# Performance work log

Hardware: AMD Instinct MI355X
Metric: run time of the kernel (lower is better)

Reference implementation:

```python
import jax, jax.numpy as jnp
import numpy as np

LN_EPS = 1e-5

def _layernorm(x, g, b):
    mu = jnp.mean(x, axis=-1, keepdims=True)
    var = jnp.mean(jnp.square(x - mu), axis=-1, keepdims=True)
    return (x - mu) * jax.lax.rsqrt(var + LN_EPS) * g + b

def setup_inputs() -> dict:
    key = jax.random.key(0)
    B, IN_DIM, S, D = 16384, 512, 32, 128
    ks = jax.random.split(key, 6)
    return {
        "x": jax.random.normal(ks[0], (B, IN_DIM), dtype=jnp.float32),
        "memory": jax.random.normal(ks[1], (1, S, D), dtype=jnp.float32),
        "ln_g": jnp.ones((IN_DIM,), dtype=jnp.float32),
        "ln_b": jnp.zeros((IN_DIM,), dtype=jnp.float32),
        "w_in": jax.random.normal(ks[2], (IN_DIM, D), dtype=jnp.float32) * 0.02,
        "b_in": jnp.zeros((D,), dtype=jnp.float32),
        "w_gate": jax.random.normal(ks[3], (2 * D, D), dtype=jnp.float32) * 0.02,
        "b_gate": jnp.zeros((D,), dtype=jnp.float32),
    }

def reference(x, memory, ln_g, ln_b, w_in, b_in, w_gate, b_gate):
    B = x.shape[0]
    mem = memory[0]                                   # [S, D]
    S, D = mem.shape
    x_proj = _layernorm(x, ln_g, ln_b) @ w_in + b_in  # [B, D]
    scores = x_proj @ mem.T                           # [B, S]
    probs = jax.nn.softmax(scores, axis=-1)           # [B, S]
    # read path
    read_content = probs @ mem                        # [B, D]
    # write path
    mem_b = jnp.broadcast_to(mem, (B, S, D))
    xp_b = jnp.broadcast_to(x_proj[:, None, :], (B, S, D))
    gate_in = jnp.concatenate([mem_b, xp_b], axis=-1)              # [B, S, 2D]
    update_gate = jax.nn.sigmoid(gate_in @ w_gate + b_gate)        # [B, S, D]
    write_info = probs[:, :, None] * x_proj[:, None, :]            # [B, S, D]
    avg_gate = jnp.mean(update_gate, axis=0, keepdims=True)        # [1, S, D]
    avg_write = jnp.mean(write_info, axis=0, keepdims=True)        # [1, S, D]
    new_memory = memory * (1.0 - avg_gate) + avg_write * avg_gate  # [1, S, D]
    return read_content, jax.lax.stop_gradient(new_memory)
```

## Files before the change

### kernel.cpp

```cpp
#include <hip/hip_runtime.h>
#include <stdint.h>

typedef __attribute__((ext_vector_type(8))) short bfrag_t;
typedef __attribute__((ext_vector_type(4))) float floatx4;

#define WFRAG_OFF   0
#define GB_OFF      294912
#define BU_OFF      311296
#define BS_OFF      311808
#define MEMFRAG_OFF 311936
#define ACC_OFF     327680
#define NBLK        512

#define M_A     0
#define M_XPF   32768
#define M_U     40960
#define M_SC    57344
#define M_PR    61440
#define M_PRT   63488
#define M_LDS   65536

__device__ __forceinline__ unsigned short f2bf(float f) {
    unsigned u = __float_as_uint(f);
    u += 0x7fffu + ((u >> 16) & 1u);
    return (unsigned short)(u >> 16);
}
__device__ __forceinline__ float sigm(float v) {
    return __builtin_amdgcn_rcpf(1.0f + __expf(-v));
}
__device__ __forceinline__ void writefrag(unsigned short* wf, int k, int n, float v) {
    int kt = k >> 5, kk = k & 31;
    int lane = (n & 15) | ((kk >> 3) << 4);
    wf[(((kt * 18) + (n >> 4)) * 64 + lane) * 8 + (kk & 7)] = f2bf(v);
}

__global__ __launch_bounds__(256) void prep_kernel(
    const float* __restrict__ memv, const float* __restrict__ w_in,
    const float* __restrict__ b_in, const float* __restrict__ w_gate,
    const float* __restrict__ b_gate, unsigned char* __restrict__ ws)
{
    int bid = blockIdx.x, t = threadIdx.x;
    unsigned short* wfrag = (unsigned short*)(ws + WFRAG_OFF);
    const float* wg2 = w_gate + 128 * 128;

    if (bid < 256) {
        __shared__ float wrow[2][128];
        int k0 = bid * 2;
        wrow[t >> 7][t & 127] = w_in[(size_t)(k0 + (t >> 7)) * 128 + (t & 127)];
        __syncthreads();
        for (int kl = 0; kl < 2; ++kl) {
            int k = k0 + kl;
            float v;
            if (t < 128) {
                v = wrow[kl][t];
            } else {
                int d = t - 128;
                float acc = 0.f;
                #pragma unroll 16
                for (int j = 0; j < 128; ++j) acc += wrow[kl][j] * wg2[j * 128 + d];
                v = acc;
            }
            writefrag(wfrag, k, t, v);
            if (t < 32) {
                float acc = 0.f;
                #pragma unroll 16
                for (int d = 0; d < 128; ++d) acc += wrow[kl][d] * memv[t * 128 + d];
                writefrag(wfrag, k, 256 + t, acc);
            }
        }
    } else if (bid < 272) {
        int idx = (bid - 256) * 256 + t;
        int s = idx >> 7, d = idx & 127;
        float acc = b_gate[d];
        #pragma unroll 16
        for (int k = 0; k < 128; ++k) acc += memv[s * 128 + k] * w_gate[k * 128 + d];
        ((float*)(ws + GB_OFF))[idx] = acc;
    } else {
        if (t < 128) {
            float acc = 0.f;
            #pragma unroll 16
            for (int j = 0; j < 128; ++j) acc += b_in[j] * wg2[j * 128 + t];
            ((float*)(ws + BU_OFF))[t] = acc;
        }
        if (t < 32) {
            float acc = 0.f;
            #pragma unroll 16
            for (int d = 0; d < 128; ++d) acc += b_in[d] * memv[t * 128 + d];
            ((float*)(ws + BS_OFF))[t] = acc;
        }
        unsigned short* mfr = (unsigned short*)(ws + MEMFRAG_OFF);
        for (int idx = t; idx < 4096; idx += 256) {
            int s = idx >> 7, d = idx & 127;
            mfr[((d >> 4) * 64 + ((d & 15) | (((s >> 3) & 3) << 4))) * 8 + (s & 7)]
                = f2bf(memv[idx]);
        }
    }
}

__global__ __launch_bounds__(512, 4) void main_kernel(
    const float* __restrict__ x,
    const float* __restrict__ ln_g, const float* __restrict__ ln_b,
    const float* __restrict__ b_in, unsigned char* __restrict__ ws,
    float* __restrict__ out)
{
    __shared__ char smem[M_LDS] __attribute__((aligned(16)));

    int tid = threadIdx.x;
    int w = tid >> 6, l = tid & 63;
    int lane_lo = l & 15, lane_hi = l >> 4;
    int row_base = blockIdx.x * 32;

    int nf = (w < 2) ? 3 : 2;
    int nts[3] = {w, w + 8, 16 + w};
    const bfrag_t* wf = (const bfrag_t*)(ws + WFRAG_OFF);

    const float4* x4 = (const float4*)x;
    float4 g0 = ((const float4*)ln_g)[l];
    float4 g1 = ((const float4*)ln_g)[l + 64];
    float4 q0 = ((const float4*)ln_b)[l];
    float4 q1 = ((const float4*)ln_b)[l + 64];

    float4 xa[4], xb[4];
    #pragma unroll
    for (int i = 0; i < 4; ++i) {
        int r = w * 4 + i;
        xa[i] = x4[(size_t)(row_base + r) * 128 + l];
        xb[i] = x4[(size_t)(row_base + r) * 128 + 64 + l];
    }

    bfrag_t bcur[3], bnxt[3], bfar[3];
    #pragma unroll
    for (int i = 0; i < 3; ++i) {
        if (i < nf) {
            bcur[i] = wf[(0 * 18 + nts[i]) * 64 + l];
            bnxt[i] = wf[(1 * 18 + nts[i]) * 64 + l];
        }
    }
    float bin_v = b_in[w * 16 + lane_lo];
    float bu_v  = ((const float*)(ws + BU_OFF))[w * 16 + lane_lo];
    float bs_v  = (w < 2) ? ((const float*)(ws + BS_OFF))[w * 16 + lane_lo] : 0.f;

    #pragma unroll
    for (int i = 0; i < 4; ++i) {
        int r = w * 4 + i;
        float s1 = xa[i].x + xa[i].y + xa[i].z + xa[i].w + xb[i].x + xb[i].y + xb[i].z + xb[i].w;
        float s2 = xa[i].x*xa[i].x + xa[i].y*xa[i].y + xa[i].z*xa[i].z + xa[i].w*xa[i].w
                 + xb[i].x*xb[i].x + xb[i].y*xb[i].y + xb[i].z*xb[i].z + xb[i].w*xb[i].w;
        #pragma unroll
        for (int m = 1; m < 64; m <<= 1) {
            s1 += __shfl_xor(s1, m);
            s2 += __shfl_xor(s2, m);
        }
        float mu = s1 * (1.f / 512.f);
        float var = s2 * (1.f / 512.f) - mu * mu;
        float rs = rsqrtf(var + 1e-5f);
        float ya0 = (xa[i].x - mu) * rs * g0.x + q0.x;
        float ya1 = (xa[i].y - mu) * rs * g0.y + q0.y;
        float ya2 = (xa[i].z - mu) * rs * g0.z + q0.z;
        float ya3 = (xa[i].w - mu) * rs * g0.w + q0.w;
        float yb0 = (xb[i].x - mu) * rs * g1.x + q1.x;
        float yb1 = (xb[i].y - mu) * rs * g1.y + q1.y;
        float yb2 = (xb[i].z - mu) * rs * g1.z + q1.z;
        float yb3 = (xb[i].w - mu) * rs * g1.w + q1.w;
        unsigned long long pa =
            (unsigned long long)f2bf(ya0) | ((unsigned long long)f2bf(ya1) << 16) |
            ((unsigned long long)f2bf(ya2) << 32) | ((unsigned long long)f2bf(ya3) << 48);
        unsigned long long pb =
            (unsigned long long)f2bf(yb0) | ((unsigned long long)f2bf(yb1) << 16) |
            ((unsigned long long)f2bf(yb2) << 32) | ((unsigned long long)f2bf(yb3) << 48);
        int sw = (r & 7) << 4;
        *(unsigned long long*)(smem + M_A + ((r * 1024 + l * 8) ^ sw)) = pa;
        *(unsigned long long*)(smem + M_A + ((r * 1024 + 512 + l * 8) ^ sw)) = pb;
    }
    __syncthreads();

    int swa = (l & 7) << 4;
    int ab0 = lane_lo * 1024 + (lane_hi << 4);
    int ab1 = (16 + lane_lo) * 1024 + (lane_hi << 4);

    floatx4 acc[3][2];
    #pragma unroll
    for (int i = 0; i < 3; ++i)
        #pragma unroll
        for (int mt = 0; mt < 2; ++mt)
            acc[i][mt] = (floatx4){0.f, 0.f, 0.f, 0.f};

    bfrag_t acur0, acur1, anxt0, anxt1, afar0, afar1;
    acur0 = *(const bfrag_t*)(smem + M_A + (ab0 ^ swa));
    acur1 = *(const bfrag_t*)(smem + M_A + (ab1 ^ swa));
    anxt0 = *(const bfrag_t*)(smem + M_A + ((ab0 + 64) ^ swa));
    anxt1 = *(const bfrag_t*)(smem + M_A + ((ab1 + 64) ^ swa));

    for (int kt = 0; kt < 16; ++kt) {
        if (kt < 14) {
            int ko = (kt + 2) * 64;
            afar0 = *(const bfrag_t*)(smem + M_A + ((ab0 + ko) ^ swa));
            afar1 = *(const bfrag_t*)(smem + M_A + ((ab1 + ko) ^ swa));
            #pragma unroll
            for (int i = 0; i < 3; ++i)
                if (i < nf) bfar[i] = wf[((kt + 2) * 18 + nts[i]) * 64 + l];
        }
        #pragma unroll
        for (int i = 0; i < 3; ++i) {
            if (i < nf) {
                acc[i][0] = __builtin_amdgcn_mfma_f32_16x16x32_bf16(acur0, bcur[i], acc[i][0], 0, 0, 0);
                acc[i][1] = __builtin_amdgcn_mfma_f32_16x16x32_bf16(acur1, bcur[i], acc[i][1], 0, 0, 0);
            }
        }
        acur0 = anxt0; acur1 = anxt1; anxt0 = afar0; anxt1 = afar1;
        #pragma unroll
        for (int i = 0; i < 3; ++i)
            if (i < nf) { bcur[i] = bnxt[i]; bnxt[i] = bfar[i]; }
    }

    {
        #pragma unroll
        for (int i = 0; i < 3; ++i) {
            if (i < nf) {
                int n = nts[i] * 16 + lane_lo;
                float bias = (i == 0) ? bin_v : ((i == 1) ? bu_v : bs_v);
                #pragma unroll
                for (int mt = 0; mt < 2; ++mt) {
                    #pragma unroll
                    for (int r4 = 0; r4 < 4; ++r4) {
                        int row = mt * 16 + lane_hi * 4 + r4;
                        float v = acc[i][mt][r4] + bias;
                        if (i == 0) {
                            int addr = M_XPF +
                                (((n >> 4) * 64 + ((n & 15) | ((row >> 3) << 4))) * 8
                                 + (row & 7)) * 2;
                            *(unsigned short*)(smem + addr) = f2bf(v);
                        } else if (i == 1) {
                            int d = n - 128;
                            *(float*)(smem + M_U + (row * 128 + d) * 4) = v;
                        } else {
                            int s = n - 256;
                            *(float*)(smem + M_SC + (row * 32 + s) * 4) = v;
                        }
                    }
                }
            }
        }
    }
    __syncthreads();

    bfrag_t bm = ((const bfrag_t*)(ws + MEMFRAG_OFF))[w * 64 + l];
    bfrag_t bx = *(const bfrag_t*)(smem + M_XPF + (w * 64 + l) * 16);
    int sbase = w * 4;
    const float* gb = (const float*)(ws + GB_OFF);
    float gbr0[4], gbr1[4];
    #pragma unroll
    for (int si = 0; si < 4; ++si) {
        gbr0[si] = gb[(sbase + si) * 128 + l];
        gbr1[si] = gb[(sbase + si) * 128 + l + 64];
    }

    #pragma unroll
    for (int i = 0; i < 4; ++i) {
        int r = w * 4 + i;
        int s = l & 31;
        float sc = *(const float*)(smem + M_SC + (r * 32 + s) * 4);
        float mx = sc;
        #pragma unroll
        for (int m = 1; m < 32; m <<= 1) mx = fmaxf(mx, __shfl_xor(mx, m));
        float e = __expf(sc - mx);
        float sum = e;
        #pragma unroll
        for (int m = 1; m < 32; m <<= 1) sum += __shfl_xor(sum, m);
        float p = e * __builtin_amdgcn_rcpf(sum);
        if (l < 32) {
            unsigned short pb = f2bf(p);
            *(unsigned short*)(smem + M_PR +
                (((r >> 4) * 64 + ((r & 15) + 16 * (s >> 3))) * 8 + (s & 7)) * 2) = pb;
            *(unsigned short*)(smem + M_PRT +
                (((s >> 4) * 64 + ((s & 15) + 16 * (r >> 3))) * 8 + (r & 7)) * 2) = pb;
        }
    }
    __syncthreads();

    float* pw = (float*)(ws + ACC_OFF + (size_t)blockIdx.x * 32768);
    {
        bfrag_t pa0 = *(const bfrag_t*)(smem + M_PR + l * 16);
        bfrag_t pa1 = *(const bfrag_t*)(smem + M_PR + 1024 + l * 16);
        bfrag_t pat0 = *(const bfrag_t*)(smem + M_PRT + l * 16);
        bfrag_t pat1 = *(const bfrag_t*)(smem + M_PRT + 1024 + l * 16);

        floatx4 r0 = (floatx4){0.f, 0.f, 0.f, 0.f};
        floatx4 r1 = (floatx4){0.f, 0.f, 0.f, 0.f};
        r0 = __builtin_amdgcn_mfma_f32_16x16x32_bf16(pa0, bm, r0, 0, 0, 0);
        r1 = __builtin_amdgcn_mfma_f32_16x16x32_bf16(pa1, bm, r1, 0, 0, 0);
        floatx4 w0 = (floatx4){0.f, 0.f, 0.f, 0.f};
        floatx4 w1 = (floatx4){0.f, 0.f, 0.f, 0.f};
        w0 = __builtin_amdgcn_mfma_f32_16x16x32_bf16(pat0, bx, w0, 0, 0, 0);
        w1 = __builtin_amdgcn_mfma_f32_16x16x32_bf16(pat1, bx, w1, 0, 0, 0);

        int nc = w * 16 + lane_lo;
        #pragma unroll
        for (int r4 = 0; r4 < 4; ++r4) {
            int row = lane_hi * 4 + r4;
            out[(size_t)(row_base + row) * 128 + nc] = r0[r4];
            out[(size_t)(row_base + row + 16) * 128 + nc] = r1[r4];
            pw[row * 128 + nc] = w0[r4];
            pw[(row + 16) * 128 + nc] = w1[r4];
        }
    }

    {
        float* pg = pw + 4096;
        float ag0[4], ag1[4];
        #pragma unroll
        for (int si = 0; si < 4; ++si) { ag0[si] = 0.f; ag1[si] = 0.f; }
        #pragma unroll 4
        for (int r = 0; r < 32; ++r) {
            float uv0 = *(const float*)(smem + M_U + (r * 128 + l) * 4);
            float uv1 = *(const float*)(smem + M_U + (r * 128 + l + 64) * 4);
            #pragma unroll
            for (int si = 0; si < 4; ++si) {
                ag0[si] += sigm(gbr0[si] + uv0);
                ag1[si] += sigm(gbr1[si] + uv1);
            }
        }
        #pragma unroll
        for (int si = 0; si < 4; ++si) {
            pg[(sbase + si) * 128 + l]      = ag0[si];
            pg[(sbase + si) * 128 + l + 64] = ag1[si];
        }
    }
}

__global__ __launch_bounds__(512) void fin_kernel(
    const float* __restrict__ memv, const unsigned char* __restrict__ ws,
    float* __restrict__ out2)
{
    __shared__ float4 red[2][32][16];
    int b = blockIdx.x, t = threadIdx.x;
    int f4 = t & 15, ch = t >> 4;
    const float* base = (const float*)(ws + ACC_OFF);
    int e4 = b * 16 + f4;

    float4 aw = {0.f, 0.f, 0.f, 0.f}, ag = {0.f, 0.f, 0.f, 0.f};
    #pragma unroll 4
    for (int c = ch * 16; c < ch * 16 + 16; ++c) {
        float4 a = ((const float4*)(base + (size_t)c * 8192))[e4];
        float4 g = ((const float4*)(base + (size_t)c * 8192 + 4096))[e4];
        aw.x += a.x; aw.y += a.y; aw.z += a.z; aw.w += a.w;
        ag.x += g.x; ag.y += g.y; ag.z += g.z; ag.w += g.w;
    }
    red[0][ch][f4] = aw;
    red[1][ch][f4] = ag;
    __syncthreads();
    if (t < 16) {
        float4 a = {0.f, 0.f, 0.f, 0.f}, g = {0.f, 0.f, 0.f, 0.f};
        #pragma unroll
        for (int c = 0; c < 32; ++c) {
            float4 ra = red[0][c][t], rg = red[1][c][t];
            a.x += ra.x; a.y += ra.y; a.z += ra.z; a.w += ra.w;
            g.x += rg.x; g.y += rg.y; g.z += rg.z; g.w += rg.w;
        }
        const float4 m4 = ((const float4*)memv)[b * 16 + t];
        float4 o;
        float s = 1.f / 16384.f;
        float gx = g.x * s, gy = g.y * s, gz = g.z * s, gw = g.w * s;
        o.x = m4.x * (1.f - gx) + a.x * s * gx;
        o.y = m4.y * (1.f - gy) + a.y * s * gy;
        o.z = m4.z * (1.f - gz) + a.z * s * gz;
        o.w = m4.w * (1.f - gw) + a.w * s * gw;
        ((float4*)out2)[b * 16 + t] = o;
    }
}

extern "C" void kernel_launch(void* const* d_in, const int* in_sizes, int n_in,
                              void* d_out, int out_size, void* d_ws, size_t ws_size,
                              hipStream_t stream)
{
    (void)in_sizes; (void)n_in; (void)out_size; (void)ws_size;
    const float* x      = (const float*)d_in[0];
    const float* memv   = (const float*)d_in[1];
    const float* ln_g   = (const float*)d_in[2];
    const float* ln_b   = (const float*)d_in[3];
    const float* w_in   = (const float*)d_in[4];
    const float* b_in   = (const float*)d_in[5];
    const float* w_gate = (const float*)d_in[6];
    const float* b_gate = (const float*)d_in[7];
    float* out = (float*)d_out;
    unsigned char* ws = (unsigned char*)d_ws;

    hipLaunchKernelGGL(prep_kernel, dim3(273), dim3(256), 0, stream,
                       memv, w_in, b_in, w_gate, b_gate, ws);
    hipLaunchKernelGGL(main_kernel, dim3(NBLK), dim3(512), 0, stream,
                       x, ln_g, ln_b, b_in, ws, out);
    hipLaunchKernelGGL(fin_kernel, dim3(64), dim3(512), 0, stream,
                       memv, ws, out + 2097152);
}
```

Before: 49.15 us.

## Store per-block partial sums as bf16 and restructure final reduction

Per-block write and gate partial accumulators are now stored as bf16 instead of fp32, halving workspace traffic between the main and final kernels. The final reduction kernel is rewritten so each thread loads one block's 16-column slice and reduces across the block with wave shuffles, using 256 blocks instead of 64. Half of the gate sigmoid accumulation loop is moved before the softmax section, likely to overlap its latency with other work. Rounding the partial sums to bf16 loses precision in the averaged memory update.

```diff
diff --git a/kernel.cpp b/kernel.cpp
--- a/kernel.cpp
+++ b/kernel.cpp
@@ -3,6 +3,7 @@
 
 typedef __attribute__((ext_vector_type(8))) short bfrag_t;
 typedef __attribute__((ext_vector_type(4))) float floatx4;
+typedef __attribute__((ext_vector_type(8))) unsigned short ushort8_t;
 
 #define WFRAG_OFF   0
 #define GB_OFF      294912
@@ -24,6 +25,9 @@
     unsigned u = __float_as_uint(f);
     u += 0x7fffu + ((u >> 16) & 1u);
     return (unsigned short)(u >> 16);
+}
+__device__ __forceinline__ float bf2f(unsigned short h) {
+    return __uint_as_float(((unsigned)h) << 16);
 }
 __device__ __forceinline__ float sigm(float v) {
     return __builtin_amdgcn_rcpf(1.0f + __expf(-v));
@@ -255,6 +259,20 @@
         gbr1[si] = gb[(sbase + si) * 128 + l + 64];
     }
 
+    float ag0[4], ag1[4];
+    #pragma unroll
+    for (int si = 0; si < 4; ++si) { ag0[si] = 0.f; ag1[si] = 0.f; }
+    #pragma unroll 4
+    for (int r = 0; r < 16; ++r) {
+        float uv0 = *(const float*)(smem + M_U + (r * 128 + l) * 4);
+        float uv1 = *(const float*)(smem + M_U + (r * 128 + l + 64) * 4);
+        #pragma unroll
+        for (int si = 0; si < 4; ++si) {
+            ag0[si] += sigm(gbr0[si] + uv0);
+            ag1[si] += sigm(gbr1[si] + uv1);
+        }
+    }
+
     #pragma unroll
     for (int i = 0; i < 4; ++i) {
         int r = w * 4 + i;
@@ -278,7 +296,7 @@
     }
     __syncthreads();
 
-    float* pw = (float*)(ws + ACC_OFF + (size_t)blockIdx.x * 32768);
+    unsigned short* pwh = (unsigned short*)(ws + ACC_OFF + (size_t)blockIdx.x * 16384);
     {
         bfrag_t pa0 = *(const bfrag_t*)(smem + M_PR + l * 16);
         bfrag_t pa1 = *(const bfrag_t*)(smem + M_PR + 1024 + l * 16);
@@ -300,18 +318,14 @@
             int row = lane_hi * 4 + r4;
             out[(size_t)(row_base + row) * 128 + nc] = r0[r4];
             out[(size_t)(row_base + row + 16) * 128 + nc] = r1[r4];
-            pw[row * 128 + nc] = w0[r4];
-            pw[(row + 16) * 128 + nc] = w1[r4];
+            pwh[row * 128 + nc] = f2bf(w0[r4]);
+            pwh[(row + 16) * 128 + nc] = f2bf(w1[r4]);
         }
     }
 
     {
-        float* pg = pw + 4096;
-        float ag0[4], ag1[4];
-        #pragma unroll
-        for (int si = 0; si < 4; ++si) { ag0[si] = 0.f; ag1[si] = 0.f; }
         #pragma unroll 4
-        for (int r = 0; r < 32; ++r) {
+        for (int r = 16; r < 32; ++r) {
             float uv0 = *(const float*)(smem + M_U + (r * 128 + l) * 4);
             float uv1 = *(const float*)(smem + M_U + (r * 128 + l + 64) * 4);
             #pragma unroll
@@ -320,10 +334,11 @@
                 ag1[si] += sigm(gbr1[si] + uv1);
             }
         }
+        unsigned short* pgh = pwh + 4096;
         #pragma unroll
         for (int si = 0; si < 4; ++si) {
-            pg[(sbase + si) * 128 + l]      = ag0[si];
-            pg[(sbase + si) * 128 + l + 64] = ag1[si];
+            pgh[(sbase + si) * 128 + l]      = f2bf(ag0[si]);
+            pgh[(sbase + si) * 128 + l + 64] = f2bf(ag1[si]);
         }
     }
 }
@@ -332,40 +347,48 @@
     const float* __restrict__ memv, const unsigned char* __restrict__ ws,
     float* __restrict__ out2)
 {
-    __shared__ float4 red[2][32][16];
+    __shared__ float red[8][32];
+    __shared__ float fsum[32];
     int b = blockIdx.x, t = threadIdx.x;
-    int f4 = t & 15, ch = t >> 4;
-    const float* base = (const float*)(ws + ACC_OFF);
-    int e4 = b * 16 + f4;
-
-    float4 aw = {0.f, 0.f, 0.f, 0.f}, ag = {0.f, 0.f, 0.f, 0.f};
-    #pragma unroll 4
-    for (int c = ch * 16; c < ch * 16 + 16; ++c) {
-        float4 a = ((const float4*)(base + (size_t)c * 8192))[e4];
-        float4 g = ((const float4*)(base + (size_t)c * 8192 + 4096))[e4];
-        aw.x += a.x; aw.y += a.y; aw.z += a.z; aw.w += a.w;
-        ag.x += g.x; ag.y += g.y; ag.z += g.z; ag.w += g.w;
-    }
-    red[0][ch][f4] = aw;
-    red[1][ch][f4] = ag;
+    int wv = t >> 6, ln = t & 63;
+    int col0 = b * 16;
+
+    const unsigned short* cb = (const unsigned short*)(ws + ACC_OFF) + (size_t)t * 8192;
+    ushort8_t a0 = *(const ushort8_t*)(cb + col0);
+    ushort8_t a1 = *(const ushort8_t*)(cb + col0 + 8);
+    ushort8_t gg0 = *(const ushort8_t*)(cb + 4096 + col0);
+    ushort8_t gg1 = *(const ushort8_t*)(cb + 4096 + col0 + 8);
+
+    float v[32];
+    #pragma unroll
+    for (int i = 0; i < 8; ++i) {
+        v[i]      = bf2f(a0[i]);
+        v[8 + i]  = bf2f(a1[i]);
+        v[16 + i] = bf2f(gg0[i]);
+        v[24 + i] = bf2f(gg1[i]);
+    }
+    #pragma unroll
+    for (int m = 1; m < 64; m <<= 1) {
+        #pragma unroll
+        for (int i = 0; i < 32; ++i) v[i] += __shfl_xor(v[i], m);
+    }
+    if (ln == 0) {
+        #pragma unroll
+        for (int i = 0; i < 32; ++i) red[wv][i] = v[i];
+    }
+    __syncthreads();
+    if (t < 32) {
+        float s = 0.f;
+        #pragma unroll
+        for (int c = 0; c < 8; ++c) s += red[c][t];
+        fsum[t] = s;
+    }
     __syncthreads();
     if (t < 16) {
-        float4 a = {0.f, 0.f, 0.f, 0.f}, g = {0.f, 0.f, 0.f, 0.f};
-        #pragma unroll
-        for (int c = 0; c < 32; ++c) {
-            float4 ra = red[0][c][t], rg = red[1][c][t];
-            a.x += ra.x; a.y += ra.y; a.z += ra.z; a.w += ra.w;
-            g.x += rg.x; g.y += rg.y; g.z += rg.z; g.w += rg.w;
-        }
-        const float4 m4 = ((const float4*)memv)[b * 16 + t];
-        float4 o;
-        float s = 1.f / 16384.f;
-        float gx = g.x * s, gy = g.y * s, gz = g.z * s, gw = g.w * s;
-        o.x = m4.x * (1.f - gx) + a.x * s * gx;
-        o.y = m4.y * (1.f - gy) + a.y * s * gy;
-        o.z = m4.z * (1.f - gz) + a.z * s * gz;
-        o.w = m4.w * (1.f - gw) + a.w * s * gw;
-        ((float4*)out2)[b * 16 + t] = o;
+        float a = fsum[t] * (1.f / 16384.f);
+        float g = fsum[16 + t] * (1.f / 16384.f);
+        int i = col0 + t;
+        out2[i] = memv[i] * (1.f - g) + a * g;
     }
 }
 
@@ -389,6 +412,6 @@
                        memv, w_in, b_in, w_gate, b_gate, ws);
     hipLaunchKernelGGL(main_kernel, dim3(NBLK), dim3(512), 0, stream,
                        x, ln_g, ln_b, b_in, ws, out);
-    hipLaunchKernelGGL(fin_kernel, dim3(64), dim3(512), 0, stream,
+    hipLaunchKernelGGL(fin_kernel, dim3(256), dim3(512), 0, stream,
                        memv, ws, out + 2097152);
 }
```

Measured after the change: 52.01 us. 1.06x slower.
